# Optimization experiments

Measured on AMD Instinct MI355X. Metric: run time of the kernel, lower is better.

The kernel has to match this reference:

```python
import jax, jax.numpy as jnp
import numpy as np

T, B, I, H, C = 4096, 32, 512, 512, 128
SCALE = 0.05  # small init keeps the relu recurrence numerically stable


def setup_inputs() -> dict:
    key = jax.random.key(0)
    ks = jax.random.split(key, 7)
    return {
        "x": jax.random.normal(ks[0], (T, B, I), dtype=jnp.float32),
        "hidden": jnp.zeros((B, H), dtype=jnp.float32),
        "W_ih": jax.random.normal(ks[1], (H, I), dtype=jnp.float32) * SCALE,
        "b_ih": jax.random.normal(ks[2], (H,), dtype=jnp.float32) * SCALE,
        "W_hh": jax.random.normal(ks[3], (H, H), dtype=jnp.float32) * SCALE,
        "b_hh": jax.random.normal(ks[4], (H,), dtype=jnp.float32) * SCALE,
        "W_fc": jax.random.normal(ks[5], (C, H), dtype=jnp.float32) * SCALE,
        "b_fc": jax.random.normal(ks[6], (C,), dtype=jnp.float32) * SCALE,
    }


def reference(x, hidden, W_ih, b_ih, W_hh, b_hh, W_fc, b_fc):
    # RNNCell (relu): h' = relu(x_t @ W_ih^T + b_ih + h @ W_hh^T + b_hh)
    def step(h, x_t):
        h_new = jax.nn.relu(x_t @ W_ih.T + b_ih + h @ W_hh.T + b_hh)
        return h_new, None

    h_final, _ = jax.lax.scan(step, hidden, x)  # scan over T timesteps
    out = h_final @ W_fc.T + b_fc  # [B, C]
    return out, h_final
```

## Files before the change

### kernel.cpp

```cpp
#include <hip/hip_runtime.h>
#include <hip/hip_bf16.h>
#include <stdint.h>

#define T_STEPS 4096
#define BATCH 32
#define IDIM 512
#define HDIM 512
#define CDIM 128
#define NSPLIT 8
#define CSLICE 64
#define QP 68

typedef float f32x4 __attribute__((ext_vector_type(4)));
typedef short s16x8 __attribute__((ext_vector_type(8)));
typedef unsigned short u16x4 __attribute__((ext_vector_type(4)));

__device__ __forceinline__ unsigned short f2bf(float f) {
    union { float f; uint32_t u; } v; v.f = f;
    uint32_t r = v.u + 0x7fffu + ((v.u >> 16) & 1u);
    return (unsigned short)(r >> 16);
}
__device__ __forceinline__ float bf2f(unsigned short s) {
    union { uint32_t u; float f; } v; v.u = ((uint32_t)s) << 16;
    return v.f;
}

__global__ void seed_hx(const float* __restrict__ h0, uint32_t* __restrict__ hx) {
    int i = blockIdx.x * 256 + threadIdx.x;
    if (i < BATCH * HDIM) {
        union { float f; uint32_t u; } v; v.f = h0[i];
        hx[i] = v.u & ~1u;
        hx[BATCH * HDIM + i] = 0x3f800001u;
    }
}

__global__ __launch_bounds__(256) void xih_gemm(
    const float* __restrict__ X,
    const float* __restrict__ Wih,
    const float* __restrict__ bih,
    const float* __restrict__ bhh,
    unsigned short* __restrict__ A)
{
    __shared__ __align__(16) unsigned short As[128][40];
    __shared__ __align__(16) unsigned short Bs[128][40];

    const int tid  = threadIdx.x;
    const int lane = tid & 63;
    const int wave = tid >> 6;
    const int wr = wave >> 1, wc = wave & 1;
    const int row0 = blockIdx.y * 128;
    const int col0 = blockIdx.x * 128;
    const int l16 = lane & 15, lhi = lane >> 4;

    const int lr = tid >> 3;
    const int kf = tid & 7;

    f32x4 acc[4][4] = {};

    for (int k0 = 0; k0 < IDIM; k0 += 32) {
        #pragma unroll
        for (int rr = 0; rr < 128; rr += 32) {
            int r = lr + rr;
            float4 xv = *(const float4*)&X[(size_t)(row0 + r) * IDIM + k0 + kf * 4];
            float4 wv = *(const float4*)&Wih[(size_t)(col0 + r) * IDIM + k0 + kf * 4];
            u16x4 xq, wq;
            xq.x = f2bf(xv.x); xq.y = f2bf(xv.y); xq.z = f2bf(xv.z); xq.w = f2bf(xv.w);
            wq.x = f2bf(wv.x); wq.y = f2bf(wv.y); wq.z = f2bf(wv.z); wq.w = f2bf(wv.w);
            *(u16x4*)&As[r][kf * 4] = xq;
            *(u16x4*)&Bs[r][kf * 4] = wq;
        }
        __syncthreads();

        s16x8 af[4], bfr[4];
        #pragma unroll
        for (int mi = 0; mi < 4; ++mi)
            af[mi] = *(const s16x8*)&As[wr * 64 + mi * 16 + l16][lhi * 8];
        #pragma unroll
        for (int ni = 0; ni < 4; ++ni)
            bfr[ni] = *(const s16x8*)&Bs[wc * 64 + ni * 16 + l16][lhi * 8];
        #pragma unroll
        for (int mi = 0; mi < 4; ++mi)
            #pragma unroll
            for (int ni = 0; ni < 4; ++ni)
                acc[mi][ni] = __builtin_amdgcn_mfma_f32_16x16x32_bf16(
                    af[mi], bfr[ni], acc[mi][ni], 0, 0, 0);
        __syncthreads();
    }

    #pragma unroll
    for (int ni = 0; ni < 4; ++ni) {
        int col = col0 + wc * 64 + ni * 16 + l16;
        float bias = bih[col] + bhh[col];
        #pragma unroll
        for (int mi = 0; mi < 4; ++mi) {
            int rowb = row0 + wr * 64 + mi * 16 + lhi * 4;
            #pragma unroll
            for (int r = 0; r < 4; ++r)
                A[(size_t)(rowb + r) * HDIM + col] = f2bf(acc[mi][ni][r] + bias);
        }
    }
}

__global__ __launch_bounds__(512, 1) void rnn_scan(
    const unsigned short* __restrict__ A,
    const float* __restrict__ Whh,
    const float* __restrict__ Wfc,
    const float* __restrict__ bfc,
    uint32_t* __restrict__ hx,
    float* __restrict__ out,
    float* __restrict__ hfin,
    int tc, int t0, int do_fc)
{
    __shared__ __align__(16) float hs[2][8 * QP];

    const int tid = threadIdx.x;
    const int b = blockIdx.x >> 3;
    const int j = blockIdx.x & 7;
    const int c = tid >> 3;
    const int q = tid & 7;
    const int cg = j * CSLICE + c;
    const int wq = (tid >> 6) * QP + (tid & 63);

    f32x4 w[16];
    {
        const float* wr = Whh + (size_t)cg * HDIM + q * 64;
        #pragma unroll
        for (int i = 0; i < 16; ++i) {
            w[i] = *(const f32x4*)(wr + i * 4);
            asm volatile("" : "+v"(w[i]));
        }
    }

    const unsigned short* Ab = A + (size_t)b * HDIM + cg;
    const uint32_t* hin_base = hx + (size_t)b * HDIM + tid;
    uint32_t* hout_base = hx + (size_t)b * HDIM + cg;

    for (int t = 0; t < tc; ++t) {
        const int gs = t0 + t;
        const uint32_t exp_tag = (uint32_t)((gs >> 1) & 1);

        float a_t = bf2f(Ab[(size_t)t * (BATCH * HDIM)]);

        const uint32_t* hp = hin_base + (size_t)(gs & 1) * (BATCH * HDIM);
        uint32_t u;
        while (((u = __hip_atomic_load(hp, __ATOMIC_RELAXED,
                                       __HIP_MEMORY_SCOPE_AGENT)) & 1u) != exp_tag) {}
        union { uint32_t u; float f; } hv_in; hv_in.u = u;
        hs[gs & 1][wq] = hv_in.f;
        __syncthreads();

        f32x4 acc = {};
        const float* hq = &hs[gs & 1][q * QP];
        #pragma unroll
        for (int i = 0; i < 16; ++i) {
            f32x4 hvv = *(const f32x4*)(hq + i * 4);
            acc += w[i] * hvv;
        }
        float v = acc.x + acc.y + acc.z + acc.w;
        v += __shfl_xor(v, 1);
        v += __shfl_xor(v, 2);
        v += __shfl_xor(v, 4);
        v = fmaxf(v + a_t, 0.f);

        if (q == 0) {
            union { float f; uint32_t u; } pv; pv.f = v;
            pv.u = (pv.u & ~1u) | (uint32_t)(((gs + 1) >> 1) & 1);
            uint32_t* ho = hout_base + (size_t)((gs + 1) & 1) * (BATCH * HDIM);
            __hip_atomic_store(ho, pv.u, __ATOMIC_RELAXED,
                               __HIP_MEMORY_SCOPE_AGENT);
            if (do_fc && t == tc - 1)
                hfin[b * HDIM + cg] = v;
        }
    }

    if (do_fc && j == 0) {
        const int target = t0 + tc;
        const uint32_t exp_tag = (uint32_t)((target >> 1) & 1);
        const uint32_t* hp = hin_base + (size_t)(target & 1) * (BATCH * HDIM);
        uint32_t u;
        while (((u = __hip_atomic_load(hp, __ATOMIC_RELAXED,
                                       __HIP_MEMORY_SCOPE_AGENT)) & 1u) != exp_tag) {}
        union { uint32_t u; float f; } hv_in; hv_in.u = u;
        hs[target & 1][wq] = hv_in.f;
        __syncthreads();

        const int c2 = tid >> 2;
        const int q2 = tid & 3;
        float facc = 0.f;
        const float* wf = Wfc + (size_t)c2 * HDIM + q2 * 128;
        const float* hb2 = hs[target & 1];
        #pragma unroll
        for (int i = 0; i < 32; ++i) {
            int e = q2 * 128 + i * 4;
            f32x4 hvv = *(const f32x4*)(hb2 + (e >> 6) * QP + (e & 63));
            f32x4 wv = *(const f32x4*)(wf + i * 4);
            f32x4 p = wv * hvv;
            facc += p.x + p.y + p.z + p.w;
        }
        facc += __shfl_xor(facc, 1);
        facc += __shfl_xor(facc, 2);
        if (q2 == 0)
            out[b * CDIM + c2] = facc + bfc[c2];
    }
}

extern "C" void kernel_launch(void* const* d_in, const int* in_sizes, int n_in,
                              void* d_out, int out_size, void* d_ws, size_t ws_size,
                              hipStream_t stream) {
    const float* x   = (const float*)d_in[0];
    const float* h0  = (const float*)d_in[1];
    const float* Wih = (const float*)d_in[2];
    const float* bih = (const float*)d_in[3];
    const float* Whh = (const float*)d_in[4];
    const float* bhh = (const float*)d_in[5];
    const float* Wfc = (const float*)d_in[6];
    const float* bfc = (const float*)d_in[7];

    float* out  = (float*)d_out;
    float* hfin = out + BATCH * CDIM;

    uint32_t* hx = (uint32_t*)d_ws;
    const size_t hx_bytes = (size_t)2 * BATCH * HDIM * sizeof(uint32_t);
    unsigned short* Abuf = (unsigned short*)((char*)d_ws + hx_bytes);

    const size_t per_t = (size_t)BATCH * HDIM * sizeof(unsigned short);
    size_t avail = ws_size > hx_bytes ? ws_size - hx_bytes : 0;
    long long tcl = (long long)(avail / per_t);
    if (tcl > T_STEPS) tcl = T_STEPS;
    int TC = (int)(tcl & ~3LL);
    if (TC < 4) TC = 4;

    seed_hx<<<(BATCH * HDIM + 255) / 256, 256, 0, stream>>>(h0, hx);

    for (int t0 = 0; t0 < T_STEPS; t0 += TC) {
        int tc = T_STEPS - t0 < TC ? T_STEPS - t0 : TC;
        xih_gemm<<<dim3(4, tc * BATCH / 128), 256, 0, stream>>>(
            x + (size_t)t0 * BATCH * IDIM, Wih, bih, bhh, Abuf);
        int do_fc = (t0 + tc >= T_STEPS) ? 1 : 0;
        rnn_scan<<<BATCH * NSPLIT, 512, 0, stream>>>(
            Abuf, Whh, Wfc, bfc, hx, out, hfin, tc, t0, do_fc);
    }
}
```

Measured before the change: 7.807 ms.

## Use inline-asm cache-scoped polling and dual stores for cross-block handoff

Replaces the agent-scope atomic load/store spin loop with hand-written global loads and stores that carry explicit cache-scope bits. Polling mostly hits a cheaper scope (sc0) and only occasionally does a device-coherent load. The producer writes both scopes so consumers on the same XCD can see updates sooner. Block-to-(batch, slice) mapping is also permuted so the 8 slices of one batch row land on different dispatch positions. The aim is lower per-step handoff latency in the serial recurrence, at the risk of relying on undocumented cache-coherence behaviour across XCDs.

```diff
diff --git a/kernel.cpp b/kernel.cpp
--- a/kernel.cpp
+++ b/kernel.cpp
@@ -23,6 +23,45 @@
 __device__ __forceinline__ float bf2f(unsigned short s) {
     union { uint32_t u; float f; } v; v.u = ((uint32_t)s) << 16;
     return v.f;
+}
+
+__device__ __forceinline__ void store_tagged(uint32_t* p, uint32_t v) {
+    uint64_t addr = (uint64_t)p;
+    asm volatile(
+        "global_store_dword %0, %1, off sc0 sc1\n\t"
+        "global_store_dword %0, %1, off sc0\n\t"
+        :: "v"(addr), "v"(v) : "memory");
+}
+
+#define FAST_POLL \
+        "global_load_dword %0, %2, off sc0\n\t" \
+        "s_waitcnt vmcnt(0)\n\t" \
+        "v_and_b32 %1, 1, %0\n\t" \
+        "v_cmp_ne_u32 vcc, %3, %1\n\t" \
+        "s_cbranch_vccz Ldone_%=\n\t"
+
+__device__ __forceinline__ uint32_t spin_tagged(const uint32_t* p, uint32_t exp_tag) {
+    uint32_t val, tmp;
+    uint64_t addr = (uint64_t)p;
+    asm volatile(
+        "global_load_dword %0, %2, off sc0 sc1\n\t"
+        "s_waitcnt vmcnt(0)\n\t"
+        "v_and_b32 %1, 1, %0\n\t"
+        "v_cmp_ne_u32 vcc, %3, %1\n\t"
+        "s_cbranch_vccz Ldone_%=\n\t"
+        "Louter_%=:\n\t"
+        FAST_POLL FAST_POLL FAST_POLL FAST_POLL
+        FAST_POLL FAST_POLL FAST_POLL FAST_POLL
+        "global_load_dword %0, %2, off sc0 sc1\n\t"
+        "s_waitcnt vmcnt(0)\n\t"
+        "v_and_b32 %1, 1, %0\n\t"
+        "v_cmp_ne_u32 vcc, %3, %1\n\t"
+        "s_cbranch_vccnz Louter_%=\n\t"
+        "Ldone_%=:\n\t"
+        : "=&v"(val), "=&v"(tmp)
+        : "v"(addr), "s"(exp_tag)
+        : "vcc", "memory");
+    return val;
 }
 
 __global__ void seed_hx(const float* __restrict__ h0, uint32_t* __restrict__ hx) {
@@ -114,8 +153,8 @@
     __shared__ __align__(16) float hs[2][8 * QP];
 
     const int tid = threadIdx.x;
-    const int b = blockIdx.x >> 3;
-    const int j = blockIdx.x & 7;
+    const int b = blockIdx.x & 31;
+    const int j = blockIdx.x >> 5;
     const int c = tid >> 3;
     const int q = tid & 7;
     const int cg = j * CSLICE + c;
@@ -142,9 +181,7 @@
         float a_t = bf2f(Ab[(size_t)t * (BATCH * HDIM)]);
 
         const uint32_t* hp = hin_base + (size_t)(gs & 1) * (BATCH * HDIM);
-        uint32_t u;
-        while (((u = __hip_atomic_load(hp, __ATOMIC_RELAXED,
-                                       __HIP_MEMORY_SCOPE_AGENT)) & 1u) != exp_tag) {}
+        uint32_t u = spin_tagged(hp, exp_tag);
         union { uint32_t u; float f; } hv_in; hv_in.u = u;
         hs[gs & 1][wq] = hv_in.f;
         __syncthreads();
@@ -166,8 +203,7 @@
             union { float f; uint32_t u; } pv; pv.f = v;
             pv.u = (pv.u & ~1u) | (uint32_t)(((gs + 1) >> 1) & 1);
             uint32_t* ho = hout_base + (size_t)((gs + 1) & 1) * (BATCH * HDIM);
-            __hip_atomic_store(ho, pv.u, __ATOMIC_RELAXED,
-                               __HIP_MEMORY_SCOPE_AGENT);
+            store_tagged(ho, pv.u);
             if (do_fc && t == tc - 1)
                 hfin[b * HDIM + cg] = v;
         }
@@ -177,9 +213,7 @@
         const int target = t0 + tc;
         const uint32_t exp_tag = (uint32_t)((target >> 1) & 1);
         const uint32_t* hp = hin_base + (size_t)(target & 1) * (BATCH * HDIM);
-        uint32_t u;
-        while (((u = __hip_atomic_load(hp, __ATOMIC_RELAXED,
-                                       __HIP_MEMORY_SCOPE_AGENT)) & 1u) != exp_tag) {}
+        uint32_t u = spin_tagged(hp, exp_tag);
         union { uint32_t u; float f; } hv_in; hv_in.u = u;
         hs[target & 1][wq] = hv_in.f;
         __syncthreads();
```

Result: slower. 22.15 ms (+183.7%).
